# Kernel tuning notes

Measured on AMD Instinct MI355X. Metric: run time of the kernel, lower is better.

## Reference

```python
import jax, jax.numpy as jnp
import numpy as np

B, S, D = 4, 2048, 1024
H, HD = 16, 64  # n_heads, head_dim (n_kv_heads == n_heads -> n_rep = 1)
WINDOW = 256
ROPE_THETA = 10000.0


def setup_inputs() -> dict:
    key = jax.random.key(0)
    ks = jax.random.split(key, 5)
    x = jax.random.normal(ks[0], (B, S, D), dtype=jnp.float32)
    scale = 0.02
    wq = jax.random.normal(ks[1], (D, D), dtype=jnp.float32) * scale
    wk = jax.random.normal(ks[2], (D, D), dtype=jnp.float32) * scale
    wv = jax.random.normal(ks[3], (D, D), dtype=jnp.float32) * scale
    wo = jax.random.normal(ks[4], (D, D), dtype=jnp.float32) * scale
    # RoPE frequencies: freqs_cis[t, i] = exp(1j * t / theta^(2i/HD)), i in [0, HD/2)
    inv_freq = 1.0 / (ROPE_THETA ** (jnp.arange(0, HD, 2, dtype=jnp.float32) / HD))
    t = jnp.arange(S, dtype=jnp.float32)
    ang = t[:, None] * inv_freq[None, :]  # [S, HD/2]
    return {"x": x, "freqs_cos": jnp.cos(ang), "freqs_sin": jnp.sin(ang),
            "wq": wq, "wk": wk, "wv": wv, "wo": wo}


def _apply_rope(xq, xk, cos, sin):
    # xq/xk: [B, S, H, HD]; cos/sin: [S, HD/2] broadcast as [1, S, 1, HD/2]
    def rot(v):
        vr = v.reshape(*v.shape[:-1], HD // 2, 2)
        v0, v1 = vr[..., 0], vr[..., 1]
        c = cos[None, :, None, :]
        s = sin[None, :, None, :]
        o0 = v0 * c - v1 * s
        o1 = v0 * s + v1 * c
        return jnp.stack([o0, o1], axis=-1).reshape(v.shape)
    return rot(xq), rot(xk)


def reference(x, freqs_cos, freqs_sin, wq, wk, wv, wo):
    b, s, _ = x.shape
    xq = (x @ wq.T).reshape(b, s, H, HD)
    xk = (x @ wk.T).reshape(b, s, H, HD)
    xv = (x @ wv.T).reshape(b, s, H, HD)
    xq, xk = _apply_rope(xq, xk, freqs_cos, freqs_sin)
    # [B, H, S, S] scores
    scores = jnp.einsum('bqhd,bkhd->bhqk', xq, xk) / jnp.sqrt(jnp.float32(HD))
    pos = jnp.arange(s)
    # masked (disallowed) when j > i (future) or i - j >= window
    bad = (pos[None, :] > pos[:, None]) | (pos[:, None] - pos[None, :] >= WINDOW)
    scores = jnp.where(bad[None, None], -jnp.inf, scores)
    attn = jax.nn.softmax(scores.astype(jnp.float32), axis=-1).astype(xq.dtype)
    out = jnp.einsum('bhqk,bkhd->bqhd', attn, xv).reshape(b, s, H * HD)
    return out @ wo.T
```

## Files before the change

### kernel.cpp

```cpp
#include <hip/hip_runtime.h>
#include <hip/hip_bf16.h>


typedef __bf16 bf16_t;
typedef __attribute__((ext_vector_type(8))) __bf16 bf16x8;
typedef __attribute__((ext_vector_type(4))) __bf16 bf16x4;
typedef __attribute__((ext_vector_type(4))) float f32x4;

#define MFMA16(a, b, c) __builtin_amdgcn_mfma_f32_16x16x32_bf16((a), (b), (c), 0, 0, 0)

__device__ __forceinline__ void async16(const void* g, void* l) {
    __builtin_amdgcn_global_load_lds(
        (const __attribute__((address_space(1))) unsigned int*)g,
        (__attribute__((address_space(3))) unsigned int*)l, 16, 0, 0);
}

#define BAR() do { asm volatile("" ::: "memory"); __builtin_amdgcn_s_barrier(); \
                   asm volatile("" ::: "memory"); } while (0)
#define VMC(N) asm volatile("s_waitcnt vmcnt(" #N ")" ::: "memory")

__global__ __launch_bounds__(256) void cvt_kernel(const float* __restrict__ s,
                                                  bf16_t* __restrict__ d, int n) {
    int i = (blockIdx.x * 256 + threadIdx.x) * 8;
    if (i >= n) return;
    float4 a = *(const float4*)(s + i);
    float4 b = *(const float4*)(s + i + 4);
    bf16x8 o;
    o[0] = (bf16_t)a.x; o[1] = (bf16_t)a.y; o[2] = (bf16_t)a.z; o[3] = (bf16_t)a.w;
    o[4] = (bf16_t)b.x; o[5] = (bf16_t)b.y; o[6] = (bf16_t)b.z; o[7] = (bf16_t)b.w;
    *(bf16x8*)(d + i) = o;
}

template <typename OUT>
__global__ __launch_bounds__(512, 1) __attribute__((amdgpu_waves_per_eu(2)))
void gemm192(const bf16_t* __restrict__ A, const bf16_t* __restrict__ Bw,
             OUT* __restrict__ C, int M, int N, int K) {
    __shared__ __attribute__((aligned(16))) bf16_t As[32768];
    __shared__ __attribute__((aligned(16))) bf16_t Bs[24576];
    const int tid = threadIdx.x;
    const int l = tid & 63, w = tid >> 6;
    const int lr = l & 15, lg = l >> 4;
    const int wr = w >> 2, wc = w & 3;

    const int nwg = gridDim.x * gridDim.y;
    const int flat = blockIdx.y * gridDim.x + blockIdx.x;
    const int swz = (flat & 7) * (nwg >> 3) + (flat >> 3);
    const int bx = swz % gridDim.x, by = swz / gridDim.x;
    const long m0 = (long)by * 256, n0 = (long)bx * 192;
    const int NT = K >> 6;
    const int NI = NT >> 1;

    const int p  = w * 1024 + l * 16;
    const int pp = p ^ (((p >> 9) & 1) << 5);
    const int st = pp >> 10;
    const int rSt = (st >> 1) * 16 + ((pp >> 6) & 15);
    const int cSt = (st & 1) * 32 + ((pp >> 4) & 3) * 8;
    const bf16_t* aS = A  + (m0 + rSt) * K + cSt;
    const bf16_t* bS = Bw + (n0 + rSt) * K + cSt;
    const long uK = 64L * K;

    auto stageA = [&](int b, int u, int t) {
        async16(aS + (long)u * uK + (long)t * 64,
                (char*)As + b * 32768 + u * 8192 + w * 1024);
    };
    auto stageB = [&](int b, int u, int t) {
        async16(bS + (long)u * uK + (long)t * 64,
                (char*)Bs + b * 24576 + u * 8192 + w * 1024);
    };

    f32x4 acc[8][3] = {};
    bf16x8 afX[4], afY[4], bfX[3], bfY[3];
    const int swd = (lr & 8) << 2;

    auto loadAF = [&](int b, int mh, int ks, bf16x8 (&dst)[4]) {
#pragma unroll
        for (int mi = 0; mi < 4; ++mi) {
            const int off = (wr * 2 + mh) * 8192 + (mi * 2 + ks) * 1024 +
                            lr * 64 + lg * 16;
            dst[mi] = *(const bf16x8*)((const char*)As + b * 32768 + (off ^ swd));
        }
    };
    auto loadBF = [&](int b, int ks, bf16x8 (&dst)[3]) {
#pragma unroll
        for (int nj = 0; nj < 3; ++nj) {
            const int rg = wc * 48 + nj * 16 + lr;
            const int off = (rg >> 6) * 8192 + (((rg >> 4) & 3) * 2 + ks) * 1024 +
                            lr * 64 + lg * 16;
            dst[nj] = *(const bf16x8*)((const char*)Bs + b * 24576 + (off ^ swd));
        }
    };

#define QMM(MH, AF, BF) do {                                                   \
    __builtin_amdgcn_s_setprio(1);                                             \
    _Pragma("unroll")                                                          \
    for (int mi = 0; mi < 4; ++mi)                                             \
        _Pragma("unroll")                                                      \
        for (int nj = 0; nj < 3; ++nj)                                         \
            acc[(MH)*4+mi][nj] = MFMA16((AF)[mi], (BF)[nj], acc[(MH)*4+mi][nj]); \
    __builtin_amdgcn_s_setprio(0);                                             \
} while (0)

    stageA(0, 0, 0); stageA(0, 1, 0); stageA(0, 2, 0); stageA(0, 3, 0);
    stageB(0, 0, 0); stageB(0, 1, 0); stageB(0, 2, 0);
    stageB(1, 0, 1); stageB(1, 1, 1); stageB(1, 2, 1);
    VMC(3);
    BAR();

#pragma unroll 1
    for (int it = 0; it < NI - 1; ++it) {
        const int T = 2 * it;
        loadAF(0, 0, 0, afX); loadBF(0, 0, bfX);
        stageA(1, 0, T + 1); stageA(1, 1, T + 1);
        BAR(); QMM(0, afX, bfX); BAR();
        loadAF(0, 1, 0, afY);
        stageA(1, 2, T + 1); stageA(1, 3, T + 1);
        BAR(); QMM(1, afY, bfX); BAR();
        loadAF(0, 0, 1, afX); loadBF(0, 1, bfY);
        BAR(); QMM(0, afX, bfY); BAR();
        loadAF(0, 1, 1, afY);
        stageB(0, 0, T + 2);
        BAR(); QMM(1, afY, bfY); VMC(1); BAR();
        loadAF(1, 0, 0, afX); loadBF(1, 0, bfX);
        stageB(0, 1, T + 2); stageB(0, 2, T + 2);
        BAR(); QMM(0, afX, bfX); BAR();
        loadAF(1, 1, 0, afY);
        stageA(0, 0, T + 2); stageA(0, 1, T + 2);
        BAR(); QMM(1, afY, bfX); BAR();
        loadAF(1, 0, 1, afX); loadBF(1, 1, bfY);
        stageA(0, 2, T + 2); stageA(0, 3, T + 2);
        BAR(); QMM(0, afX, bfY); BAR();
        loadAF(1, 1, 1, afY);
        stageB(1, 0, T + 3); stageB(1, 1, T + 3); stageB(1, 2, T + 3);
        BAR(); QMM(1, afY, bfY); VMC(3); BAR();
    }

    {
        loadAF(0, 0, 0, afX); loadBF(0, 0, bfX);
        stageA(1, 0, NT - 1); stageA(1, 1, NT - 1);
        BAR(); QMM(0, afX, bfX); BAR();
        loadAF(0, 1, 0, afY);
        stageA(1, 2, NT - 1); stageA(1, 3, NT - 1);
        BAR(); QMM(1, afY, bfX); BAR();
        loadAF(0, 0, 1, afX); loadBF(0, 1, bfY);
        BAR(); QMM(0, afX, bfY); BAR();
        loadAF(0, 1, 1, afY);
        BAR(); QMM(1, afY, bfY);
        VMC(0); BAR();
        loadAF(1, 0, 0, afX); loadBF(1, 0, bfX);
        QMM(0, afX, bfX);
        loadAF(1, 1, 0, afY);
        QMM(1, afY, bfX);
        loadAF(1, 0, 1, afX); loadBF(1, 1, bfY);
        QMM(0, afX, bfY);
        loadAF(1, 1, 1, afY);
        QMM(1, afY, bfY);
    }
#undef QMM

#pragma unroll
    for (int ai = 0; ai < 8; ++ai)
#pragma unroll
        for (int nj = 0; nj < 3; ++nj)
#pragma unroll
            for (int j = 0; j < 4; ++j) {
                long r = m0 + wr * 128 + ai * 16 + lg * 4 + j;
                long c = n0 + wc * 48 + nj * 16 + lr;
                C[r * (long)N + c] = (OUT)acc[ai][nj][j];
            }
}

template <typename OUT>
__global__ __launch_bounds__(512, 2) void gemm256(const bf16_t* __restrict__ A,
                                                  const bf16_t* __restrict__ Bw,
                                                  OUT* __restrict__ C,
                                                  int M, int N, int K) {
    __shared__ __attribute__((aligned(16))) bf16_t As[49152];
    __shared__ __attribute__((aligned(16))) bf16_t Bs[24576];
    const int tid = threadIdx.x;
    const int l = tid & 63, w = tid >> 6;
    const int lr = l & 15, lg = l >> 4;
    const int wr = w >> 1, wc = w & 1;

    const int nwg = gridDim.x * gridDim.y;
    const int flat = blockIdx.y * gridDim.x + blockIdx.x;
    const int swz = (flat & 7) * (nwg >> 3) + (flat >> 3);
    const int bx = swz % gridDim.x, by = swz / gridDim.x;
    const long m0 = (long)by * 256, n0 = (long)bx * 128;
    const int NT = K >> 6;

    int rS[2], cS[2];
#pragma unroll
    for (int i = 0; i < 2; ++i) {
        const int p  = i * 8192 + w * 1024 + l * 16;
        const int pp = p ^ (((p >> 9) & 1) << 5);
        const int st = pp >> 10;
        rS[i] = (st >> 1) * 16 + ((pp >> 6) & 15);
        cS[i] = (st & 1) * 32 + ((pp >> 4) & 3) * 8;
    }
    const bf16_t* aSrc0 = A  + (m0 + rS[0]) * K + cS[0];
    const bf16_t* aSrc1 = A  + (m0 + rS[1]) * K + cS[1];
    const bf16_t* bSrc0 = Bw + (n0 + rS[0]) * K + cS[0];
    const bf16_t* bSrc1 = Bw + (n0 + rS[1]) * K + cS[1];
    const long hK = 128L * K;

    auto stageA = [&](int b, int h, int t) {
        char* d = (char*)As + b * 32768 + h * 16384 + w * 1024;
        const long o = (long)h * hK + (long)t * 64;
        async16(aSrc0 + o, d);
        async16(aSrc1 + o, d + 8192);
    };
    auto stageB = [&](int b, int t) {
        char* d = (char*)Bs + b * 16384 + w * 1024;
        const long o = (long)t * 64;
        async16(bSrc0 + o, d);
        async16(bSrc1 + o, d + 8192);
    };

    f32x4 acc[4][4] = {};
    bf16x8 af[4][2], blo[2][2], bhi[2][2];
    const int swd = (lr & 8) << 2;

    auto loadA = [&](int b) {
#pragma unroll
        for (int mi = 0; mi < 4; ++mi)
#pragma unroll
            for (int ks = 0; ks < 2; ++ks) {
                const int ra = (wr & 1) * 64 + mi * 16 + lr;
                const int off = ((ra >> 4) * 2 + ks) * 1024 + (ra & 15) * 64 + lg * 16;
                af[mi][ks] = *(const bf16x8*)((const char*)As + b * 32768 +
                                              (wr >> 1) * 16384 + (off ^ swd));
            }
    };
    auto loadB = [&](int b, int nh, bf16x8 (&dst)[2][2]) {
#pragma unroll
        for (int nj = 0; nj < 2; ++nj)
#pragma unroll
            for (int ks = 0; ks < 2; ++ks) {
                const int rb = wc * 64 + (nh * 2 + nj) * 16 + lr;
                const int off = ((rb >> 4) * 2 + ks) * 1024 + (rb & 15) * 64 + lg * 16;
                dst[nj][ks] = *(const bf16x8*)((const char*)Bs + b * 16384 +
                                               (off ^ swd));
            }
    };

#define QMM(NH, BF) do {                                                       \
    __builtin_amdgcn_s_setprio(1);                                             \
    _Pragma("unroll")                                                          \
    for (int mi = 0; mi < 4; ++mi) {                                           \
        acc[mi][(NH)*2]   = MFMA16(af[mi][0], (BF)[0][0], acc[mi][(NH)*2]);    \
        acc[mi][(NH)*2]   = MFMA16(af[mi][1], (BF)[0][1], acc[mi][(NH)*2]);    \
        acc[mi][(NH)*2+1] = MFMA16(af[mi][0], (BF)[1][0], acc[mi][(NH)*2+1]);  \
        acc[mi][(NH)*2+1] = MFMA16(af[mi][1], (BF)[1][1], acc[mi][(NH)*2+1]);  \
    }                                                                          \
    __builtin_amdgcn_s_setprio(0);                                             \
} while (0)

    stageA(0, 0, 0); stageA(0, 1, 0); stageB(0, 0);
    stageA(1, 0, 1); stageA(1, 1, 1); stageB(1, 1);
    VMC(6);
    BAR();

    int bc = 0;
#pragma unroll 1
    for (int t = 0; t < NT - 2; ++t) {
        const int bn = (bc + 2 >= 3) ? bc - 1 : bc + 2;
        loadA(bc); loadB(bc, 0, blo); stageA(bn, 0, t + 2); stageA(bn, 1, t + 2);
        BAR(); QMM(0, blo); BAR();
        loadB(bc, 1, bhi); stageB(bn, t + 2);
        BAR(); QMM(1, bhi);
        if (t < NT - 3) { VMC(6); } else { VMC(0); }
        BAR();
        bc = (bc + 1 >= 3) ? 0 : bc + 1;
    }
    {
        loadA(bc); loadB(bc, 0, blo);
        QMM(0, blo);
        loadB(bc, 1, bhi);
        QMM(1, bhi);
        const int b2 = (bc + 1 >= 3) ? 0 : bc + 1;
        loadA(b2); loadB(b2, 0, blo);
        QMM(0, blo);
        loadB(b2, 1, bhi);
        QMM(1, bhi);
    }
#undef QMM

#pragma unroll
    for (int mi = 0; mi < 4; ++mi)
#pragma unroll
        for (int ni = 0; ni < 4; ++ni)
#pragma unroll
            for (int j = 0; j < 4; ++j) {
                long r = m0 + wr * 64 + mi * 16 + lg * 4 + j;
                long c = n0 + wc * 64 + ni * 16 + lr;
                C[r * (long)N + c] = (OUT)acc[mi][ni][j];
            }
}

__global__ __launch_bounds__(256) void rope_reshape(const bf16_t* __restrict__ Cq,
                                                    const float* __restrict__ fcos,
                                                    const float* __restrict__ fsin,
                                                    bf16_t* __restrict__ Qo,
                                                    bf16_t* __restrict__ Ko,
                                                    bf16_t* __restrict__ VT) {
    __shared__ __attribute__((aligned(16))) bf16_t vt[64][72];
    const int blk = blockIdx.x;
    const int st = blk & 31, bh = blk >> 5;
    const int h = bh & 15, b = bh >> 4;
    const int s0 = st << 6;
    const int tid = threadIdx.x;
    const int i = tid >> 2, dq = (tid & 3) << 4;
    const int s = s0 + i;

    const bf16_t* base = Cq + (long)(b * 2048 + s) * 3072 + h * 64 + dq;
    bf16x8 q0v = *(const bf16x8*)(base);
    bf16x8 q1v = *(const bf16x8*)(base + 8);
    bf16x8 k0v = *(const bf16x8*)(base + 1024);
    bf16x8 k1v = *(const bf16x8*)(base + 1032);
    bf16x8 v0v = *(const bf16x8*)(base + 2048);
    bf16x8 v1v = *(const bf16x8*)(base + 2056);

    float cs[8], sn[8];
    {
        const float* cp = fcos + (long)s * 32 + (dq >> 1);
        const float* sp = fsin + (long)s * 32 + (dq >> 1);
        float4 a = *(const float4*)cp, b2 = *(const float4*)(cp + 4);
        float4 c = *(const float4*)sp, d2 = *(const float4*)(sp + 4);
        cs[0]=a.x; cs[1]=a.y; cs[2]=a.z; cs[3]=a.w; cs[4]=b2.x; cs[5]=b2.y; cs[6]=b2.z; cs[7]=b2.w;
        sn[0]=c.x; sn[1]=c.y; sn[2]=c.z; sn[3]=c.w; sn[4]=d2.x; sn[5]=d2.y; sn[6]=d2.z; sn[7]=d2.w;
    }

    auto rope8 = [&](bf16x8 v, int fo) -> bf16x8 {
        bf16x8 o;
#pragma unroll
        for (int p = 0; p < 4; ++p) {
            float v0 = (float)v[2 * p], v1 = (float)v[2 * p + 1];
            float c = cs[fo + p], s2 = sn[fo + p];
            o[2 * p]     = (bf16_t)(v0 * c - v1 * s2);
            o[2 * p + 1] = (bf16_t)(v0 * s2 + v1 * c);
        }
        return o;
    };

    bf16x8 qo0 = rope8(q0v, 0), qo1 = rope8(q1v, 4);
    bf16x8 ko0 = rope8(k0v, 0), ko1 = rope8(k1v, 4);

    const long qaddr = ((long)bh * 2048 + s) * 64 + dq;
    *(bf16x8*)(Qo + qaddr) = qo0;
    *(bf16x8*)(Qo + qaddr + 8) = qo1;
    *(bf16x8*)(Ko + qaddr) = ko0;
    *(bf16x8*)(Ko + qaddr + 8) = ko1;

    *(bf16x8*)&vt[i][dq] = v0v;
    *(bf16x8*)&vt[i][dq + 8] = v1v;
    __syncthreads();
    const int d = tid >> 2, sb = (tid & 3) << 4;
    bf16x8 o0, o1;
#pragma unroll
    for (int j = 0; j < 8; ++j) {
        const int f = ((j & 3) << 1) | ((j >> 2) & 1);
        o0[j] = vt[sb + f][d];
        o1[j] = vt[sb + 8 + f][d];
    }
    const long va = ((long)bh * 64 + d) * 2048 + s0 + sb;
    *(bf16x8*)(VT + va) = o0;
    *(bf16x8*)(VT + va + 8) = o1;
}

__global__ __launch_bounds__(256, 2) void attn_win4(const bf16_t* __restrict__ Q,
                                                    const bf16_t* __restrict__ Kb,
                                                    const bf16_t* __restrict__ VT,
                                                    bf16_t* __restrict__ Ao) {
    __shared__ __attribute__((aligned(16))) bf16_t kld[5 * 4096];
    __shared__ __attribute__((aligned(16))) bf16_t vld[5 * 4096];
    const int raw = blockIdx.x;
    const int mswz = ((raw & 7) << 8) | (raw >> 3);
    const int qt = mswz & 31, bh = mswz >> 5;
    const int h = bh & 15, b = bh >> 4;
    const int l = threadIdx.x & 63, w = threadIdx.x >> 6;
    const int lr = l & 15, lg = l >> 4;
    const int q0 = qt * 64 + w * 16;
    const int q = q0 + lr;
    const int tb = qt - 4;

    const bf16_t* Qp = Q + (long)bh * 2048 * 64;
    const bf16_t* Kp = Kb + (long)bh * 2048 * 64;
    const bf16_t* Vp = VT + (long)bh * 64 * 2048;

#pragma unroll
    for (int u = 0; u < 5; ++u) {
        const int kt = tb + u;
        const int kt64 = (kt < 0 ? 0 : kt) * 64;
#pragma unroll
        for (int part = 0; part < 2; ++part) {
            const int seg = w * 2 + part;
            const int r = seg * 8 + (l >> 3);
            const int sc = (l & 7) ^ ((r >> 1) & 7);
            async16(Kp + (long)(kt64 + r) * 64 + sc * 8,
                    (char*)kld + u * 8192 + seg * 1024);
            async16(Vp + (long)r * 2048 + kt64 + sc * 8,
                    (char*)vld + u * 8192 + seg * 1024);
        }
    }

    const bf16x8 qb0 = *(const bf16x8*)&Qp[q * 64 + lg * 8];
    const bf16x8 qb1 = *(const bf16x8*)&Qp[q * 64 + 32 + lg * 8];

    __syncthreads();

    float mrun = -1000.f, lsum = 0.f;
    f32x4 o0 = {0.f, 0.f, 0.f, 0.f}, o1 = {0.f, 0.f, 0.f, 0.f};
    f32x4 o2 = {0.f, 0.f, 0.f, 0.f}, o3 = {0.f, 0.f, 0.f, 0.f};
    const int swv = (lr >> 1) & 7;

#define QKF(DST, HH, MM)                                                         \
    f32x4 DST; {                                                                 \
        const int row_ = (HH) * 32 + 2 * lr + (MM);                              \
        const int sw_ = (row_ >> 1) & 7;                                         \
        bf16x8 k0_ = *(const bf16x8*)(kbase + row_ * 128 + ((lg ^ sw_) << 4));   \
        bf16x8 k1_ = *(const bf16x8*)(kbase + row_ * 128 + (((4 + lg) ^ sw_) << 4)); \
        f32x4 s_ = {0.f, 0.f, 0.f, 0.f};                                         \
        s_ = MFMA16(k0_, qb0, s_);                                               \
        s_ = MFMA16(k1_, qb1, s_);                                               \
        const int kb_ = k0s + (HH) * 32 + (MM) + lg * 8;                         \
        DST[0] = ((kb_ >= 0) & ((unsigned)(q - kb_) < 256u))         ? s_[0] * 0.125f : -1e30f; \
        DST[1] = ((kb_ + 2 >= 0) & ((unsigned)(q - kb_ - 2) < 256u)) ? s_[1] * 0.125f : -1e30f; \
        DST[2] = ((kb_ + 4 >= 0) & ((unsigned)(q - kb_ - 4) < 256u)) ? s_[2] * 0.125f : -1e30f; \
        DST[3] = ((kb_ + 6 >= 0) & ((unsigned)(q - kb_ - 6) < 256u)) ? s_[3] * 0.125f : -1e30f; \
    }

#define EXV(S_) {                                                                \
        S_[0] = __expf(S_[0] - mnew); S_[1] = __expf(S_[1] - mnew);              \
        S_[2] = __expf(S_[2] - mnew); S_[3] = __expf(S_[3] - mnew);              \
        rs += (S_[0] + S_[1]) + (S_[2] + S_[3]); }

#define PVF(NT, HH, PB) {                                                        \
        bf16x8 va_ = *(const bf16x8*)(vbase + ((NT) * 16 + lr) * 128 +           \
                                      ((((HH) * 4 + lg) ^ swv) << 4));           \
        o##NT = MFMA16(va_, PB, o##NT); }

#pragma unroll
    for (int u = 0; u < 5; ++u) {
        const char* kbase = (const char*)kld + u * 8192;
        const char* vbase = (const char*)vld + u * 8192;
        const int k0s = (tb + u) * 64;

        QKF(sA, 0, 0) QKF(sB, 0, 1) QKF(sC, 1, 0) QKF(sD, 1, 1)

        float tm = fmaxf(fmaxf(fmaxf(sA[0], sA[1]), fmaxf(sA[2], sA[3])),
                         fmaxf(fmaxf(sB[0], sB[1]), fmaxf(sB[2], sB[3])));
        tm = fmaxf(tm, fmaxf(fmaxf(fmaxf(sC[0], sC[1]), fmaxf(sC[2], sC[3])),
                             fmaxf(fmaxf(sD[0], sD[1]), fmaxf(sD[2], sD[3]))));
        tm = fmaxf(tm, __shfl_xor(tm, 16));
        tm = fmaxf(tm, __shfl_xor(tm, 32));
        const float mnew = fmaxf(mrun, tm);
        const float alpha = __expf(mrun - mnew);
        mrun = mnew;

        float rs = 0.f;
        EXV(sA) EXV(sB) EXV(sC) EXV(sD)
        rs += __shfl_xor(rs, 16);
        rs += __shfl_xor(rs, 32);
        lsum = lsum * alpha + rs;

        o0[0] *= alpha; o0[1] *= alpha; o0[2] *= alpha; o0[3] *= alpha;
        o1[0] *= alpha; o1[1] *= alpha; o1[2] *= alpha; o1[3] *= alpha;
        o2[0] *= alpha; o2[1] *= alpha; o2[2] *= alpha; o2[3] *= alpha;
        o3[0] *= alpha; o3[1] *= alpha; o3[2] *= alpha; o3[3] *= alpha;

        bf16x8 pb0, pb1;
        pb0[0] = (bf16_t)sA[0]; pb0[1] = (bf16_t)sA[1]; pb0[2] = (bf16_t)sA[2]; pb0[3] = (bf16_t)sA[3];
        pb0[4] = (bf16_t)sB[0]; pb0[5] = (bf16_t)sB[1]; pb0[6] = (bf16_t)sB[2]; pb0[7] = (bf16_t)sB[3];
        pb1[0] = (bf16_t)sC[0]; pb1[1] = (bf16_t)sC[1]; pb1[2] = (bf16_t)sC[2]; pb1[3] = (bf16_t)sC[3];
        pb1[4] = (bf16_t)sD[0]; pb1[5] = (bf16_t)sD[1]; pb1[6] = (bf16_t)sD[2]; pb1[7] = (bf16_t)sD[3];

        PVF(0, 0, pb0) PVF(1, 0, pb0) PVF(2, 0, pb0) PVF(3, 0, pb0)
        PVF(0, 1, pb1) PVF(1, 1, pb1) PVF(2, 1, pb1) PVF(3, 1, pb1)
    }
#undef QKF
#undef EXV
#undef PVF

    const float rinv = 1.0f / lsum;
    bf16_t* aor = Ao + ((long)(b * 2048) + q) * 1024 + h * 64;
#define EPI(NT, OA_) {                                                           \
        bf16x4 ov_;                                                             \
        ov_[0] = (bf16_t)(OA_[0] * rinv); ov_[1] = (bf16_t)(OA_[1] * rinv);      \
        ov_[2] = (bf16_t)(OA_[2] * rinv); ov_[3] = (bf16_t)(OA_[3] * rinv);      \
        *(bf16x4*)(aor + (NT) * 16 + lg * 4) = ov_; }
    EPI(0, o0) EPI(1, o1) EPI(2, o2) EPI(3, o3)
#undef EPI
}

extern "C" void kernel_launch(void* const* d_in, const int* in_sizes, int n_in,
                              void* d_out, int out_size, void* d_ws, size_t ws_size,
                              hipStream_t stream) {
    (void)in_sizes; (void)n_in; (void)out_size; (void)ws_size;
    const float* x    = (const float*)d_in[0];
    const float* fcos = (const float*)d_in[1];
    const float* fsin = (const float*)d_in[2];
    const float* wq   = (const float*)d_in[3];
    const float* wk   = (const float*)d_in[4];
    const float* wv   = (const float*)d_in[5];
    const float* wo   = (const float*)d_in[6];
    float* out = (float*)d_out;

    char* ws = (char*)d_ws;
    bf16_t* xbf  = (bf16_t*)(ws);
    bf16_t* wqkv = (bf16_t*)(ws + 16777216);
    bf16_t* wobf = (bf16_t*)(ws + 23068672);
    bf16_t* qkvc = (bf16_t*)(ws + 25165824);
    bf16_t* kbuf = (bf16_t*)(ws + 75497472);
    bf16_t* vtb  = (bf16_t*)(ws + 92274688);
    bf16_t* qbuf = xbf;
    bf16_t* aob  = qkvc;

    cvt_kernel<<<4096, 256, 0, stream>>>(x, xbf, 8388608);
    cvt_kernel<<<512, 256, 0, stream>>>(wq, wqkv, 1048576);
    cvt_kernel<<<512, 256, 0, stream>>>(wk, wqkv + 1048576, 1048576);
    cvt_kernel<<<512, 256, 0, stream>>>(wv, wqkv + 2097152, 1048576);
    cvt_kernel<<<512, 256, 0, stream>>>(wo, wobf, 1048576);

    gemm192<bf16_t><<<dim3(16, 32), 512, 0, stream>>>(xbf, wqkv, qkvc, 8192, 3072, 1024);
    rope_reshape<<<2048, 256, 0, stream>>>(qkvc, fcos, fsin, qbuf, kbuf, vtb);
    attn_win4<<<2048, 256, 0, stream>>>(qbuf, kbuf, vtb, aob);
    gemm256<float><<<dim3(8, 32), 512, 0, stream>>>(aob, wobf, out, 8192, 1024, 1024);
}
```

Baseline: 143.0 us.

## Simplify GEMM pipelines to double-buffered one-barrier-per-tile loops and shrink LDS

```diff
diff --git a/kernel.cpp b/kernel.cpp
--- a/kernel.cpp
+++ b/kernel.cpp
@@ -48,7 +48,6 @@
     const int bx = swz % gridDim.x, by = swz / gridDim.x;
     const long m0 = (long)by * 256, n0 = (long)bx * 192;
     const int NT = K >> 6;
-    const int NI = NT >> 1;
 
     const int p  = w * 1024 + l * 16;
     const int pp = p ^ (((p >> 9) & 1) << 5);
@@ -102,57 +101,33 @@
 
     stageA(0, 0, 0); stageA(0, 1, 0); stageA(0, 2, 0); stageA(0, 3, 0);
     stageB(0, 0, 0); stageB(0, 1, 0); stageB(0, 2, 0);
-    stageB(1, 0, 1); stageB(1, 1, 1); stageB(1, 2, 1);
-    VMC(3);
-    BAR();
+    VMC(0); BAR();
 
 #pragma unroll 1
-    for (int it = 0; it < NI - 1; ++it) {
-        const int T = 2 * it;
-        loadAF(0, 0, 0, afX); loadBF(0, 0, bfX);
-        stageA(1, 0, T + 1); stageA(1, 1, T + 1);
-        BAR(); QMM(0, afX, bfX); BAR();
-        loadAF(0, 1, 0, afY);
-        stageA(1, 2, T + 1); stageA(1, 3, T + 1);
-        BAR(); QMM(1, afY, bfX); BAR();
-        loadAF(0, 0, 1, afX); loadBF(0, 1, bfY);
-        BAR(); QMM(0, afX, bfY); BAR();
-        loadAF(0, 1, 1, afY);
-        stageB(0, 0, T + 2);
-        BAR(); QMM(1, afY, bfY); VMC(1); BAR();
-        loadAF(1, 0, 0, afX); loadBF(1, 0, bfX);
-        stageB(0, 1, T + 2); stageB(0, 2, T + 2);
-        BAR(); QMM(0, afX, bfX); BAR();
-        loadAF(1, 1, 0, afY);
-        stageA(0, 0, T + 2); stageA(0, 1, T + 2);
-        BAR(); QMM(1, afY, bfX); BAR();
-        loadAF(1, 0, 1, afX); loadBF(1, 1, bfY);
-        stageA(0, 2, T + 2); stageA(0, 3, T + 2);
-        BAR(); QMM(0, afX, bfY); BAR();
-        loadAF(1, 1, 1, afY);
-        stageB(1, 0, T + 3); stageB(1, 1, T + 3); stageB(1, 2, T + 3);
-        BAR(); QMM(1, afY, bfY); VMC(3); BAR();
-    }
-
+    for (int t = 0; t < NT - 1; ++t) {
+        const int bc = t & 1, bn = bc ^ 1;
+        loadAF(bc, 0, 0, afX); loadBF(bc, 0, bfX);
+        stageA(bn, 0, t + 1); stageA(bn, 1, t + 1);
+        stageA(bn, 2, t + 1); stageA(bn, 3, t + 1);
+        stageB(bn, 0, t + 1); stageB(bn, 1, t + 1); stageB(bn, 2, t + 1);
+        loadAF(bc, 1, 0, afY);
+        QMM(0, afX, bfX);
+        loadAF(bc, 0, 1, afX); loadBF(bc, 1, bfY);
+        QMM(1, afY, bfX);
+        loadAF(bc, 1, 1, afY);
+        QMM(0, afX, bfY);
+        QMM(1, afY, bfY);
+        VMC(0); BAR();
+    }
     {
-        loadAF(0, 0, 0, afX); loadBF(0, 0, bfX);
-        stageA(1, 0, NT - 1); stageA(1, 1, NT - 1);
-        BAR(); QMM(0, afX, bfX); BAR();
-        loadAF(0, 1, 0, afY);
-        stageA(1, 2, NT - 1); stageA(1, 3, NT - 1);
-        BAR(); QMM(1, afY, bfX); BAR();
-        loadAF(0, 0, 1, afX); loadBF(0, 1, bfY);
-        BAR(); QMM(0, afX, bfY); BAR();
-        loadAF(0, 1, 1, afY);
-        BAR(); QMM(1, afY, bfY);
-        VMC(0); BAR();
-        loadAF(1, 0, 0, afX); loadBF(1, 0, bfX);
+        const int bc = (NT - 1) & 1;
+        loadAF(bc, 0, 0, afX); loadBF(bc, 0, bfX);
+        loadAF(bc, 1, 0, afY);
         QMM(0, afX, bfX);
-        loadAF(1, 1, 0, afY);
+        loadAF(bc, 0, 1, afX); loadBF(bc, 1, bfY);
         QMM(1, afY, bfX);
-        loadAF(1, 0, 1, afX); loadBF(1, 1, bfY);
+        loadAF(bc, 1, 1, afY);
         QMM(0, afX, bfY);
-        loadAF(1, 1, 1, afY);
         QMM(1, afY, bfY);
     }
 #undef QMM
@@ -174,8 +149,8 @@
                                                   const bf16_t* __restrict__ Bw,
                                                   OUT* __restrict__ C,
                                                   int M, int N, int K) {
-    __shared__ __attribute__((aligned(16))) bf16_t As[49152];
-    __shared__ __attribute__((aligned(16))) bf16_t Bs[24576];
+    __shared__ __attribute__((aligned(16))) bf16_t As[32768];
+    __shared__ __attribute__((aligned(16))) bf16_t Bs[16384];
     const int tid = threadIdx.x;
     const int l = tid & 63, w = tid >> 6;
     const int lr = l & 15, lg = l >> 4;
@@ -256,31 +231,23 @@
 } while (0)
 
     stageA(0, 0, 0); stageA(0, 1, 0); stageB(0, 0);
-    stageA(1, 0, 1); stageA(1, 1, 1); stageB(1, 1);
-    VMC(6);
-    BAR();
-
-    int bc = 0;
+    VMC(0); BAR();
+
 #pragma unroll 1
-    for (int t = 0; t < NT - 2; ++t) {
-        const int bn = (bc + 2 >= 3) ? bc - 1 : bc + 2;
-        loadA(bc); loadB(bc, 0, blo); stageA(bn, 0, t + 2); stageA(bn, 1, t + 2);
-        BAR(); QMM(0, blo); BAR();
-        loadB(bc, 1, bhi); stageB(bn, t + 2);
-        BAR(); QMM(1, bhi);
-        if (t < NT - 3) { VMC(6); } else { VMC(0); }
-        BAR();
-        bc = (bc + 1 >= 3) ? 0 : bc + 1;
+    for (int t = 0; t < NT - 1; ++t) {
+        const int bc = t & 1, bn = bc ^ 1;
+        loadA(bc); loadB(bc, 0, blo);
+        stageA(bn, 0, t + 1); stageA(bn, 1, t + 1); stageB(bn, t + 1);
+        loadB(bc, 1, bhi);
+        QMM(0, blo);
+        QMM(1, bhi);
+        VMC(0); BAR();
     }
     {
+        const int bc = (NT - 1) & 1;
         loadA(bc); loadB(bc, 0, blo);
+        loadB(bc, 1, bhi);
         QMM(0, blo);
-        loadB(bc, 1, bhi);
-        QMM(1, bhi);
-        const int b2 = (bc + 1 >= 3) ? 0 : bc + 1;
-        loadA(b2); loadB(b2, 0, blo);
-        QMM(0, blo);
-        loadB(b2, 1, bhi);
         QMM(1, bhi);
     }
 #undef QMM
@@ -293,7 +260,7 @@
             for (int j = 0; j < 4; ++j) {
                 long r = m0 + wr * 64 + mi * 16 + lg * 4 + j;
                 long c = n0 + wc * 64 + ni * 16 + lr;
-                C[r * (long)N + c] = (OUT)acc[mi][ni][j];
+                C[r * N + c] = (OUT)acc[mi][ni][j];
             }
 }
 
```

Result: slower. 153.6 us (+7.5%).
